# Performance work log

Hardware: AMD Instinct MI355X
Metric: run time of the kernel (lower is better)

## Reference

```python
import jax, jax.numpy as jnp
import numpy as np

B, C, NQ, NK, S, H, FF = 8, 256, 1024, 4096, 16, 8, 2048
DH = C // H
EPS = 1e-5


def _layernorm(x, g, b):
    m = jnp.mean(x, axis=-1, keepdims=True)
    v = jnp.mean((x - m) ** 2, axis=-1, keepdims=True)
    return (x - m) * jax.lax.rsqrt(v + EPS) * g + b


def _box_query(key_pos, query_pos):
    # key_pos: (B,NK,3); query_pos: (B,NQ,6) = centers ++ box sizes (L,H,W)
    centers = query_pos[:, :, None, :3]            # (B,NQ,1,3)
    half = 0.5 * query_pos[:, :, None, 3:]         # (B,NQ,1,3)
    off = jnp.abs(key_pos[:, None, :, :] - centers)  # (B,NQ,NK,3)
    inside = jnp.all(off <= half, axis=-1)         # (B,NQ,NK)
    # first n_sample inside-points in index order (stable sort: inside first)
    order = jnp.argsort(~inside, axis=-1, stable=True)
    idx = order[..., :S]                           # (B,NQ,S)
    valid = jnp.take_along_axis(inside, idx, axis=-1)
    mask = ~valid                                  # True = padded / masked
    idx = jnp.where(mask, 0, idx)
    mask = mask.at[..., 0].set(False)              # matches cuda path: slot 0 never masked
    return idx, mask


def _forward(query, key, query_pos, key_pos,
             q_w, q_b, k_w, k_b, v_w, v_b, o_w, o_b,
             lin1_w, lin1_b, lin2_w, lin2_b,
             n1_g, n1_b, n2_g, n2_b, qpe_w, qpe_b, kpe_w, kpe_b):
    idx, mask = _box_query(key_pos, query_pos)     # (B,NQ,S), (B,NQ,S)
    # gather neighborhoods
    gxyz = jax.vmap(lambda kp, ix: kp[ix])(key_pos, idx)        # (B,NQ,S,3)
    gxyz = gxyz - query_pos[:, :, None, :3]                     # center-relative
    gfeat = jax.vmap(lambda kf, ix: kf[:, ix])(key, idx)        # (B,C,NQ,S)

    BQ = B * NQ
    kfeat = jnp.transpose(gfeat, (0, 2, 3, 1)).reshape(BQ, S, C)   # (BQ,S,C)
    kpe = gxyz.reshape(BQ, S, 3) @ kpe_w.T + kpe_b                 # cross_embed
    qtok = jnp.transpose(query, (0, 2, 1)).reshape(BQ, C)          # (BQ,C)
    qpe = (query_pos @ qpe_w.T + qpe_b).reshape(BQ, C)             # pos_embed

    # multihead cross-attention: 1 query vs S=16 local keys per group
    kv_in = kfeat + kpe
    qh = ((qtok + qpe) @ q_w.T + q_b).reshape(BQ, H, DH)
    kh = (kv_in @ k_w.T + k_b).reshape(BQ, S, H, DH)
    vh = (kv_in @ v_w.T + v_b).reshape(BQ, S, H, DH)
    scores = jnp.einsum('bhd,bshd->bhs', qh, kh) / np.sqrt(DH)    # (BQ,H,S)
    scores = jnp.where(mask.reshape(BQ, 1, S), -1e30, scores)
    attn = jax.nn.softmax(scores, axis=-1)
    ao = jnp.einsum('bhs,bshd->bhd', attn, vh).reshape(BQ, C)
    ao = ao @ o_w.T + o_b

    x = _layernorm(qtok + ao, n1_g, n1_b)                         # post-norm
    ff = jax.nn.relu(x @ lin1_w.T + lin1_b) @ lin2_w.T + lin2_b
    x = _layernorm(x + ff, n2_g, n2_b)
    return jnp.transpose(x.reshape(B, NQ, C), (0, 2, 1))          # (B,C,NQ)


def setup_inputs() -> dict:
    rng = jax.random.key(0)
    ks = jax.random.split(rng, 24)
    s = 0.02
    query = jax.random.normal(ks[0], (B, C, NQ), jnp.float32)
    key = jax.random.normal(ks[1], (B, C, NK), jnp.float32)
    key_pos = jax.random.uniform(ks[2], (B, NK, 3), jnp.float32)
    centers = jax.random.uniform(ks[3], (B, NQ, 3), jnp.float32)
    sizes = jax.random.uniform(ks[4], (B, NQ, 3), jnp.float32, minval=0.1, maxval=0.4)
    query_pos = jnp.concatenate([centers, sizes], axis=-1)
    p = {
        'q_w': jax.random.normal(ks[5], (C, C)) * s, 'q_b': jnp.zeros((C,)),
        'k_w': jax.random.normal(ks[6], (C, C)) * s, 'k_b': jnp.zeros((C,)),
        'v_w': jax.random.normal(ks[7], (C, C)) * s, 'v_b': jnp.zeros((C,)),
        'o_w': jax.random.normal(ks[8], (C, C)) * s, 'o_b': jnp.zeros((C,)),
        'lin1_w': jax.random.normal(ks[9], (FF, C)) * s, 'lin1_b': jnp.zeros((FF,)),
        'lin2_w': jax.random.normal(ks[10], (C, FF)) * s, 'lin2_b': jnp.zeros((C,)),
        'n1_g': jnp.ones((C,)), 'n1_b': jnp.zeros((C,)),
        'n2_g': jnp.ones((C,)), 'n2_b': jnp.zeros((C,)),
        'qpe_w': jax.random.normal(ks[11], (C, 6)) * s, 'qpe_b': jnp.zeros((C,)),
        'kpe_w': jax.random.normal(ks[12], (C, 3)) * s, 'kpe_b': jnp.zeros((C,)),
    }
    return dict(query=query, key=key, query_pos=query_pos, key_pos=key_pos, **p)


def reference(query, key, query_pos, key_pos,
              q_w, q_b, k_w, k_b, v_w, v_b, o_w, o_b,
              lin1_w, lin1_b, lin2_w, lin2_b,
              n1_g, n1_b, n2_g, n2_b, qpe_w, qpe_b, kpe_w, kpe_b):
    return _forward(query, key, query_pos, key_pos,
                    q_w, q_b, k_w, k_b, v_w, v_b, o_w, o_b,
                    lin1_w, lin1_b, lin2_w, lin2_b,
                    n1_g, n1_b, n2_g, n2_b, qpe_w, qpe_b, kpe_w, kpe_b)
```

## Files before the change

### kernel.cpp

```cpp
#include <hip/hip_runtime.h>
#include <cstdint>

#define B_   8
#define C_   256
#define NQ_  1024
#define NK_  4096
#define S_   16
#define H_   8
#define FF_  2048
#define DH_  32
#define BQ_  (B_*NQ_)
#define EPS_ 1e-5f
#define KS_  8

typedef __bf16 bf16x8 __attribute__((ext_vector_type(8)));
typedef __bf16 bf16x4 __attribute__((ext_vector_type(4)));
typedef float  f32x4  __attribute__((ext_vector_type(4)));

struct CvtArgs {
  const float* src[6];
  __bf16* dst[6];
};

#define SEGA 2048
#define SEGB 10240
#define SEGC 12288
#define SEGD 13568
#define NPREP 13584

__global__ __launch_bounds__(256) void k_prep(
    const float* __restrict__ query, const float* __restrict__ key,
    const float* __restrict__ query_pos, const float* __restrict__ key_pos,
    const float* __restrict__ qpe_w, const float* __restrict__ qpe_b,
    const float* __restrict__ k_w, const float* __restrict__ k_b,
    const float* __restrict__ v_w, const float* __restrict__ v_b,
    const float* __restrict__ kpe_w, const float* __restrict__ kpe_b,
    CvtArgs ca,
    __bf16* __restrict__ keyTb, __bf16* __restrict__ qtokb,
    __bf16* __restrict__ qinb,
    float4* __restrict__ Pk, float4* __restrict__ Pv,
    int* __restrict__ idxo, int* __restrict__ masko) {
  __shared__ __align__(16) float smem[1248];
  int blk = blockIdx.x, t = threadIdx.x;
  int tx = t & 31, ty = t >> 5;

  if (blk < SEGA) {
    int lane = t & 63;
    int q = blk * 4 + (t >> 6);
    int b = q >> 10;
    const float* kpb = key_pos + (size_t)b * NK_ * 3;
    const float* qp = query_pos + (size_t)q * 6;
    float cx = qp[0], cy = qp[1], cz = qp[2];
    float hx = 0.5f * qp[3], hy = 0.5f * qp[4], hz = 0.5f * qp[5];
    int* iq = idxo + (size_t)q * S_;
    int found = 0;
    for (int ch = 0; ch < NK_ / 64; ch += 4) {
      float dx[4], dy[4], dz[4];
#pragma unroll
      for (int u = 0; u < 4; ++u) {
        int k = (ch + u) * 64 + lane;
        dx[u] = fabsf(kpb[k * 3 + 0] - cx);
        dy[u] = fabsf(kpb[k * 3 + 1] - cy);
        dz[u] = fabsf(kpb[k * 3 + 2] - cz);
      }
#pragma unroll
      for (int u = 0; u < 4; ++u) {
        bool inside = (dx[u] <= hx) && (dy[u] <= hy) && (dz[u] <= hz);
        unsigned long long bal = __ballot(inside);
        if (inside) {
          int slot = found + __popcll(bal & ((1ull << lane) - 1ull));
          if (slot < S_) iq[slot] = (ch + u) * 64 + lane;
        }
        found += __popcll(bal);
      }
      if (found >= S_) break;
    }
    if (found > S_) found = S_;
    if (lane < S_) {
      int m = (lane < found) ? 0 : 1;
      if (lane >= found) iq[lane] = 0;
      if (lane == 0) m = 0;
      masko[(size_t)q * S_ + lane] = m;
    }
  } else if (blk < SEGB) {
    int local = blk - SEGA;
    float (*tt)[33] = (float(*)[33])smem;
    int x = local & 127, y = (local >> 7) & 7, z = local >> 10;
    int j0 = x * 32, i0 = y * 32;
    const float* inz = key + (size_t)z * C_ * NK_;
    __bf16* outz = keyTb + (size_t)z * NK_ * C_;
#pragma unroll
    for (int r = 0; r < 32; r += 8)
      tt[ty + r][tx] = inz[(size_t)(i0 + ty + r) * NK_ + (j0 + tx)];
    __syncthreads();
#pragma unroll
    for (int r = 0; r < 32; r += 8)
      outz[(size_t)(j0 + ty + r) * C_ + (i0 + tx)] = (__bf16)tt[tx][ty + r];
  } else if (blk < SEGC) {
    int local = blk - SEGB;
    float (*tt)[33] = (float(*)[33])smem;
    float (*sqp)[6] = (float(*)[6])(smem + 1056);
    int x = local & 31, y = (local >> 5) & 7, z = local >> 8;
    int nq0 = x * 32, c0 = y * 32;
    const float* inz = query + (size_t)z * C_ * NQ_;
#pragma unroll
    for (int r = 0; r < 32; r += 8)
      tt[ty + r][tx] = inz[(size_t)(c0 + ty + r) * NQ_ + (nq0 + tx)];
    if (t < 192)
      sqp[t / 6][t % 6] = query_pos[((size_t)z * NQ_ + nq0 + t / 6) * 6 + (t % 6)];
    int c = c0 + tx;
    float w0 = qpe_w[c * 6 + 0], w1 = qpe_w[c * 6 + 1], w2 = qpe_w[c * 6 + 2];
    float w3 = qpe_w[c * 6 + 3], w4 = qpe_w[c * 6 + 4], w5 = qpe_w[c * 6 + 5];
    float wb = qpe_b[c];
    __syncthreads();
#pragma unroll
    for (int r = 0; r < 32; r += 8) {
      int nql = ty + r;
      size_t row = (size_t)z * NQ_ + nq0 + nql;
      float v = tt[tx][nql];
      float pe = wb + sqp[nql][0] * w0 + sqp[nql][1] * w1 + sqp[nql][2] * w2 +
                 sqp[nql][3] * w3 + sqp[nql][4] * w4 + sqp[nql][5] * w5;
      qtokb[row * C_ + c] = (__bf16)v;
      qinb[row * C_ + c] = (__bf16)(v + pe);
    }
  } else if (blk < SEGD) {
    int local = blk - SEGC;
    int idx, base;
    if (local < 64)       { idx = 0; base = local; }
    else if (local < 128) { idx = 1; base = local - 64; }
    else if (local < 192) { idx = 2; base = local - 128; }
    else if (local < 256) { idx = 3; base = local - 192; }
    else if (local < 768) { idx = 4; base = local - 256; }
    else                  { idx = 5; base = local - 768; }
    size_t off = (size_t)base * 1024 + t * 4;
    float4 v = *(const float4*)(ca.src[idx] + off);
    __bf16* o = ca.dst[idx] + off;
    o[0] = (__bf16)v.x; o[1] = (__bf16)v.y; o[2] = (__bf16)v.z; o[3] = (__bf16)v.w;
  } else {
    int local = blk - SEGD;
    int bx = local & 7, bv = local >> 3;
    const float* w  = bv ? v_w : k_w;
    const float* wb = bv ? v_b : k_b;
    float4* P = bv ? Pv : Pk;
    float4 (*red)[8] = (float4(*)[8])smem;
    int nl = t >> 3, ks = (t & 7) * 32;
    int n = bx * 32 + nl;
    const float* wr = w + (size_t)n * C_;
    float p0 = 0.f, p1 = 0.f, p2 = 0.f, pb = 0.f;
#pragma unroll
    for (int k = ks; k < ks + 32; ++k) {
      float wv = wr[k];
      p0 += kpe_w[k * 3 + 0] * wv;
      p1 += kpe_w[k * 3 + 1] * wv;
      p2 += kpe_w[k * 3 + 2] * wv;
      pb += kpe_b[k] * wv;
    }
    red[nl][t & 7] = make_float4(p0, p1, p2, pb);
    __syncthreads();
    if (t < 32) {
      float4 s = red[t][0];
#pragma unroll
      for (int j = 1; j < 8; ++j) {
        float4 r = red[t][j];
        s.x += r.x; s.y += r.y; s.z += r.z; s.w += r.w;
      }
      s.w += wb[bx * 32 + t];
      P[bx * 32 + t] = s;
    }
  }
}

template <int BM, int BN, int RELU, int OUT_BF16>
__device__ __forceinline__ void gemm_body(
    const __bf16* __restrict__ A, const __bf16* __restrict__ Wn,
    const float* __restrict__ bias, void* __restrict__ outp,
    int n0, int m0, int N, int K, int kbeg, int kend) {
  constexpr int MI = BM / 32, JN = BN / 32;
  constexpr int AIT = (BM * 64) / 2048, BIT = (BN * 64) / 2048;
  __shared__ __bf16 As[BM][72];
  __shared__ __bf16 Bs[BN][72];
  int t = threadIdx.x;
  int lane = t & 63, w = t >> 6;
  int lane16 = lane & 15, quad = lane >> 4;
  int wm = (w & 1) * (BM / 2), wn = (w >> 1) * (BN / 2);

  f32x4 acc[MI][JN];
#pragma unroll
  for (int i = 0; i < MI; ++i)
#pragma unroll
    for (int j = 0; j < JN; ++j) acc[i][j] = (f32x4){0.f, 0.f, 0.f, 0.f};

  for (int k0 = kbeg; k0 < kend; k0 += 64) {
#pragma unroll
    for (int i = 0; i < AIT; ++i) {
      int ii = i * 256 + t;
      int m = ii >> 3, kc = (ii & 7) * 8;
      *(bf16x8*)&As[m][kc] = *(const bf16x8*)&A[(size_t)(m0 + m) * K + k0 + kc];
    }
#pragma unroll
    for (int i = 0; i < BIT; ++i) {
      int ii = i * 256 + t;
      int m = ii >> 3, kc = (ii & 7) * 8;
      *(bf16x8*)&Bs[m][kc] = *(const bf16x8*)&Wn[(size_t)(n0 + m) * K + k0 + kc];
    }
    __syncthreads();
#pragma unroll
    for (int kk = 0; kk < 64; kk += 32) {
      bf16x8 af[MI], bfr[JN];
#pragma unroll
      for (int i = 0; i < MI; ++i)
        af[i] = *(const bf16x8*)&As[wm + i * 16 + lane16][kk + quad * 8];
#pragma unroll
      for (int j = 0; j < JN; ++j)
        bfr[j] = *(const bf16x8*)&Bs[wn + j * 16 + lane16][kk + quad * 8];
#pragma unroll
      for (int i = 0; i < MI; ++i)
#pragma unroll
        for (int j = 0; j < JN; ++j)
          acc[i][j] = __builtin_amdgcn_mfma_f32_16x16x32_bf16(af[i], bfr[j], acc[i][j], 0, 0, 0);
    }
    __syncthreads();
  }

#pragma unroll
  for (int j = 0; j < JN; ++j) {
    int col = n0 + wn + j * 16 + lane16;
    float bv = bias ? bias[col] : 0.f;
#pragma unroll
    for (int i = 0; i < MI; ++i) {
#pragma unroll
      for (int r = 0; r < 4; ++r) {
        int row = m0 + wm + i * 16 + quad * 4 + r;
        float v = acc[i][j][r] + bv;
        if (RELU) v = fmaxf(v, 0.f);
        if (OUT_BF16)
          ((__bf16*)outp)[(size_t)row * N + col] = (__bf16)v;
        else
          ((float*)outp)[(size_t)row * N + col] = v;
      }
    }
  }
}

template <int BM, int BN, int RELU, int OUT_BF16>
__global__ __launch_bounds__(256) void k_gemm(
    const __bf16* __restrict__ A, const __bf16* __restrict__ Wn,
    const float* __restrict__ bias, void* __restrict__ outp, int N, int K) {
  gemm_body<BM, BN, RELU, OUT_BF16>(A, Wn, bias, outp,
                                    blockIdx.x * BN, blockIdx.y * BM, N, K, 0, K);
}

__global__ __launch_bounds__(256) void k_gemmsk(
    const __bf16* __restrict__ A, const __bf16* __restrict__ Wn,
    __bf16* __restrict__ partials) {
  int ks = blockIdx.z;
  int kbeg = ks * (FF_ / KS_), kend = kbeg + FF_ / KS_;
  gemm_body<128, 128, 0, 1>(A, Wn, nullptr,
                            partials + (size_t)ks * BQ_ * C_,
                            blockIdx.x * 128, blockIdx.y * 128, C_, FF_, kbeg, kend);
}

__global__ __launch_bounds__(256) void k_gemmsko(
    const __bf16* __restrict__ A, const __bf16* __restrict__ Wn,
    __bf16* __restrict__ partials) {
  int ks = blockIdx.z;
  int kbeg = ks * 128, kend = kbeg + 128;
  gemm_body<128, 64, 0, 1>(A, Wn, nullptr,
                           partials + (size_t)ks * BQ_ * C_,
                           blockIdx.x * 64, blockIdx.y * 128, C_, C_, kbeg, kend);
}

__global__ __launch_bounds__(256) void k_gemm2(
    const __bf16* __restrict__ keyTb, const __bf16* __restrict__ kvwb,
    __bf16* __restrict__ khvbuf,
    const __bf16* __restrict__ qinb, const __bf16* __restrict__ qwb,
    const float* __restrict__ q_b, __bf16* __restrict__ qhb) {
  int blk = blockIdx.x;
  const __bf16 *A, *Wn; const float* bias; __bf16* outp; int n0, m0, N;
  if (blk < 128) {
    A = qinb; Wn = qwb; bias = q_b; outp = qhb;
    n0 = (blk & 1) * 128; m0 = (blk >> 1) * 128; N = 256;
  } else {
    int l = blk - 128;
    A = keyTb; Wn = kvwb; bias = nullptr; outp = khvbuf;
    n0 = (l & 3) * 128; m0 = (l >> 2) * 128; N = 512;
  }
  gemm_body<128, 128, 0, 1>(A, Wn, bias, outp, n0, m0, N, 256, 0, 256);
}

__global__ __launch_bounds__(256) void k_attnf(
    const __bf16* __restrict__ khv,
    const float* __restrict__ key_pos,
    const float* __restrict__ query_pos,
    const int* __restrict__ idx,
    const int* __restrict__ maskb,
    const __bf16* __restrict__ qhb,
    const float4* __restrict__ Pk,
    const float4* __restrict__ Pv,
    __bf16* __restrict__ aob) {
  __shared__ __bf16 kvs[S_][520];
  __shared__ float qrow[C_];
  __shared__ float sc[H_][S_];
  __shared__ float pw[H_][S_];
  __shared__ float4 gx4[S_];
  __shared__ float4 pgxs[H_];
  __shared__ float4 qpks[H_];
  __shared__ int srow[S_], smask[S_];
  int bq = blockIdx.x, b = bq >> 10, t = threadIdx.x;

  if (t < S_) {
    int k = idx[(size_t)bq * S_ + t];
    srow[t] = b * NK_ + k;
    smask[t] = maskb[(size_t)bq * S_ + t];
    const float* kpp = key_pos + ((size_t)b * NK_ + k) * 3;
    const float* qp  = query_pos + (size_t)bq * 6;
    gx4[t] = make_float4(kpp[0] - qp[0], kpp[1] - qp[1], kpp[2] - qp[2], 1.f);
  }
  float qv_t = (float)qhb[(size_t)bq * C_ + t];
  qrow[t] = qv_t;
  {
    float4 p = Pk[t];
    p.x *= qv_t; p.y *= qv_t; p.z *= qv_t; p.w *= qv_t;
#pragma unroll
    for (int off = 16; off >= 1; off >>= 1) {
      p.x += __shfl_xor(p.x, off);
      p.y += __shfl_xor(p.y, off);
      p.z += __shfl_xor(p.z, off);
      p.w += __shfl_xor(p.w, off);
    }
    if ((t & 31) == 0) {
      const float s = 0.17677669529663687f;
      qpks[t >> 5] = make_float4(p.x * s, p.y * s, p.z * s, p.w * s);
    }
  }
  __syncthreads();
  {
    int s = t >> 4, c0 = (t & 15) * 32;
    const __bf16* src = khv + (size_t)srow[s] * 512 + c0;
    *(bf16x8*)&kvs[s][c0]      = *(const bf16x8*)&src[0];
    *(bf16x8*)&kvs[s][c0 + 8]  = *(const bf16x8*)&src[8];
    *(bf16x8*)&kvs[s][c0 + 16] = *(const bf16x8*)&src[16];
    *(bf16x8*)&kvs[s][c0 + 24] = *(const bf16x8*)&src[24];
  }
  __syncthreads();
  if (t < H_ * S_) {
    int h = t >> 4, s = t & (S_ - 1);
    float d = 0.f;
#pragma unroll
    for (int c0 = 0; c0 < 32; c0 += 8) {
      bf16x8 xv = *(const bf16x8*)&kvs[s][h * 32 + c0];
#pragma unroll
      for (int j = 0; j < 8; ++j) d += qrow[h * 32 + c0 + j] * (float)xv[j];
    }
    d *= 0.17677669529663687f;
    float4 g = gx4[s];
    float4 pk = qpks[h];
    d += g.x * pk.x + g.y * pk.y + g.z * pk.z + pk.w;
    if (smask[s]) d = -1e30f;
    sc[h][s] = d;
  }
  __syncthreads();
  if (t < H_) {
    float mx = -3.4e38f;
#pragma unroll
    for (int s = 0; s < S_; ++s) mx = fmaxf(mx, sc[t][s]);
    float e[S_], sum = 0.f;
#pragma unroll
    for (int s = 0; s < S_; ++s) { e[s] = expf(sc[t][s] - mx); sum += e[s]; }
    float inv = 1.f / sum;
    float gxx = 0.f, gyy = 0.f, gzz = 0.f;
#pragma unroll
    for (int s = 0; s < S_; ++s) {
      float p = e[s] * inv;
      pw[t][s] = p;
      float4 g = gx4[s];
      gxx += p * g.x; gyy += p * g.y; gzz += p * g.z;
    }
    pgxs[t] = make_float4(gxx, gyy, gzz, 1.f);
  }
  __syncthreads();
  {
    int h = t >> 5;
    float a = 0.f;
#pragma unroll
    for (int s = 0; s < S_; ++s) a += pw[h][s] * (float)kvs[s][256 + t];
    float4 pv = Pv[t];
    float4 g = pgxs[h];
    a += g.x * pv.x + g.y * pv.y + g.z * pv.z + pv.w;
    aob[(size_t)bq * C_ + t] = (__bf16)a;
  }
}

__global__ __launch_bounds__(256) void k_ln1(const __bf16* __restrict__ xa,
                                             const __bf16* __restrict__ op2,
                                             const float* __restrict__ obias,
                                             const float* __restrict__ g,
                                             const float* __restrict__ bb,
                                             __bf16* __restrict__ outb) {
  int wid = (blockIdx.x * 256 + threadIdx.x) >> 6;
  int lane = threadIdx.x & 63;
  bf16x4 va = *(const bf16x4*)&xa[(size_t)wid * C_ + lane * 4];
  float4 ob4 = *(const float4*)(obias + lane * 4);
  bf16x4 p0 = *(const bf16x4*)&op2[(size_t)wid * C_ + lane * 4];
  bf16x4 p1 = *(const bf16x4*)&op2[(size_t)BQ_ * C_ + (size_t)wid * C_ + lane * 4];
  float x0 = (float)va[0] + ob4.x + (float)p0[0] + (float)p1[0];
  float x1 = (float)va[1] + ob4.y + (float)p0[1] + (float)p1[1];
  float x2 = (float)va[2] + ob4.z + (float)p0[2] + (float)p1[2];
  float x3 = (float)va[3] + ob4.w + (float)p0[3] + (float)p1[3];
  float s = x0 + x1 + x2 + x3;
#pragma unroll
  for (int off = 32; off >= 1; off >>= 1) s += __shfl_xor(s, off);
  float mean = s * (1.f / C_);
  float d0 = x0 - mean, d1 = x1 - mean, d2 = x2 - mean, d3 = x3 - mean;
  float v = d0 * d0 + d1 * d1 + d2 * d2 + d3 * d3;
#pragma unroll
  for (int off = 32; off >= 1; off >>= 1) v += __shfl_xor(v, off);
  float inv = 1.f / sqrtf(v * (1.f / C_) + EPS_);
  float4 g4 = *(const float4*)(g + lane * 4);
  float4 b4 = *(const float4*)(bb + lane * 4);
  __bf16* obp = outb + (size_t)wid * C_ + lane * 4;
  obp[0] = (__bf16)(d0 * inv * g4.x + b4.x);
  obp[1] = (__bf16)(d1 * inv * g4.y + b4.y);
  obp[2] = (__bf16)(d2 * inv * g4.z + b4.z);
  obp[3] = (__bf16)(d3 * inv * g4.w + b4.w);
}

__global__ __launch_bounds__(256) void k_lnt(const __bf16* __restrict__ x1b,
                                             const __bf16* __restrict__ ff2p,
                                             const float* __restrict__ l2bias,
                                             const float* __restrict__ g,
                                             const float* __restrict__ bb,
                                             float* __restrict__ out) {
  __shared__ float buf[32][257];
  int z = blockIdx.y, nq0 = blockIdx.x * 32;
  int t = threadIdx.x;
  int w = t >> 6, lane = t & 63;
  float4 g4 = *(const float4*)(g + lane * 4);
  float4 b4 = *(const float4*)(bb + lane * 4);
  float4 l2b = *(const float4*)(l2bias + lane * 4);
#pragma unroll
  for (int rr = 0; rr < 8; ++rr) {
    int row = w * 8 + rr;
    size_t grow = (size_t)z * NQ_ + nq0 + row;
    bf16x4 va = *(const bf16x4*)&x1b[grow * C_ + lane * 4];
    float x0 = (float)va[0] + l2b.x, x1 = (float)va[1] + l2b.y;
    float x2 = (float)va[2] + l2b.z, x3 = (float)va[3] + l2b.w;
#pragma unroll
    for (int ks = 0; ks < KS_; ++ks) {
      bf16x4 p = *(const bf16x4*)&ff2p[((size_t)ks * BQ_ + grow) * C_ + lane * 4];
      x0 += (float)p[0]; x1 += (float)p[1]; x2 += (float)p[2]; x3 += (float)p[3];
    }
    float s = x0 + x1 + x2 + x3;
#pragma unroll
    for (int off = 32; off >= 1; off >>= 1) s += __shfl_xor(s, off);
    float mean = s * (1.f / C_);
    float d0 = x0 - mean, d1 = x1 - mean, d2 = x2 - mean, d3 = x3 - mean;
    float v = d0 * d0 + d1 * d1 + d2 * d2 + d3 * d3;
#pragma unroll
    for (int off = 32; off >= 1; off >>= 1) v += __shfl_xor(v, off);
    float inv = 1.f / sqrtf(v * (1.f / C_) + EPS_);
    buf[row][lane * 4 + 0] = d0 * inv * g4.x + b4.x;
    buf[row][lane * 4 + 1] = d1 * inv * g4.y + b4.y;
    buf[row][lane * 4 + 2] = d2 * inv * g4.z + b4.z;
    buf[row][lane * 4 + 3] = d3 * inv * g4.w + b4.w;
  }
  __syncthreads();
  int tx = t & 31, ty = t >> 5;
#pragma unroll
  for (int ci = 0; ci < 32; ++ci) {
    int c = ci * 8 + ty;
    out[((size_t)z * C_ + c) * NQ_ + nq0 + tx] = buf[tx][c];
  }
}

extern "C" void kernel_launch(void* const* d_in, const int* in_sizes, int n_in,
                              void* d_out, int out_size, void* d_ws, size_t ws_size,
                              hipStream_t stream) {
  const float* query     = (const float*)d_in[0];
  const float* key       = (const float*)d_in[1];
  const float* query_pos = (const float*)d_in[2];
  const float* key_pos   = (const float*)d_in[3];
  const float* q_w = (const float*)d_in[4];  const float* q_b = (const float*)d_in[5];
  const float* k_w = (const float*)d_in[6];  const float* k_b = (const float*)d_in[7];
  const float* v_w = (const float*)d_in[8];  const float* v_b = (const float*)d_in[9];
  const float* o_w = (const float*)d_in[10]; const float* o_b = (const float*)d_in[11];
  const float* lin1_w = (const float*)d_in[12]; const float* lin1_b = (const float*)d_in[13];
  const float* lin2_w = (const float*)d_in[14]; const float* lin2_b = (const float*)d_in[15];
  const float* n1_g = (const float*)d_in[16]; const float* n1_b = (const float*)d_in[17];
  const float* n2_g = (const float*)d_in[18]; const float* n2_b = (const float*)d_in[19];
  const float* qpe_w = (const float*)d_in[20]; const float* qpe_b = (const float*)d_in[21];
  const float* kpe_w = (const float*)d_in[22]; const float* kpe_b = (const float*)d_in[23];
  float* out = (float*)d_out;

  const size_t BQc = (size_t)BQ_ * C_;
  float* w = (float*)d_ws;
  size_t o = 0;
  __bf16* keyTb = (__bf16*)(w + o); o += (size_t)B_ * NK_ * C_ / 2;
  __bf16* qtokb = (__bf16*)(w + o); o += BQc / 2;
  __bf16* op2  = (__bf16*)(w + o); o += BQc;
  __bf16* khvbuf = (__bf16*)(w + o); o += (size_t)B_ * NK_ * 512 / 2;
  __bf16* ff2p = (__bf16*)(w + o); o += BQc * KS_ / 2;
  __bf16* qinb = (__bf16*)(w + o); o += BQc / 2;
  __bf16* qhb  = (__bf16*)(w + o); o += BQc / 2;
  __bf16* aob  = (__bf16*)(w + o); o += BQc / 2;
  __bf16* x1b  = (__bf16*)(w + o); o += BQc / 2;
  __bf16* qwb  = (__bf16*)(w + o); o += (size_t)C_ * C_ / 2;
  __bf16* kvwb = (__bf16*)(w + o); o += (size_t)C_ * C_;
  __bf16* owb  = (__bf16*)(w + o); o += (size_t)C_ * C_ / 2;
  __bf16* l1b  = (__bf16*)(w + o); o += (size_t)C_ * FF_ / 2;
  __bf16* l2b  = (__bf16*)(w + o); o += (size_t)C_ * FF_ / 2;
  float4* Pk   = (float4*)(w + o); o += C_ * 4;
  float4* Pv   = (float4*)(w + o); o += C_ * 4;
  int* idxb  = (int*)(w + o); o += (size_t)BQ_ * S_;
  int* maskb = (int*)(w + o); o += (size_t)BQ_ * S_;
  __bf16* ff1b = khvbuf;

  CvtArgs ca;
  ca.src[0] = q_w; ca.dst[0] = qwb;
  ca.src[1] = k_w; ca.dst[1] = kvwb;
  ca.src[2] = v_w; ca.dst[2] = kvwb + (size_t)C_ * C_;
  ca.src[3] = o_w; ca.dst[3] = owb;
  ca.src[4] = lin1_w; ca.dst[4] = l1b;
  ca.src[5] = lin2_w; ca.dst[5] = l2b;
  k_prep<<<NPREP, 256, 0, stream>>>(query, key, query_pos, key_pos,
                                    qpe_w, qpe_b, k_w, k_b, v_w, v_b,
                                    kpe_w, kpe_b, ca,
                                    keyTb, qtokb, qinb, Pk, Pv, idxb, maskb);
  k_gemm2<<<128 + 1024, 256, 0, stream>>>(keyTb, kvwb, khvbuf, qinb, qwb, q_b, qhb);
  k_attnf<<<BQ_, 256, 0, stream>>>(khvbuf, key_pos, query_pos, idxb, maskb,
                                   qhb, Pk, Pv, aob);
  k_gemmsko<<<dim3(C_ / 64, BQ_ / 128, 2), 256, 0, stream>>>(aob, owb, op2);
  k_ln1<<<BQ_ / 4, 256, 0, stream>>>(qtokb, op2, o_b, n1_g, n1_b, x1b);
  k_gemm<128, 128, 1, 1><<<dim3(FF_ / 128, BQ_ / 128), 256, 0, stream>>>(
      x1b, l1b, lin1_b, ff1b, FF_, C_);
  k_gemmsk<<<dim3(C_ / 128, BQ_ / 128, KS_), 256, 0, stream>>>(ff1b, l2b, ff2p);
  k_lnt<<<dim3(NQ_ / 32, B_), 256, 0, stream>>>(x1b, ff2p, lin2_b, n2_g, n2_b, out);
}
```

Measured before the change: 259.5 us.

## Fuse split-K GEMM reductions with LayerNorm via last-block atomic counters

Merges the output-projection split-K GEMM with the first LayerNorm, and the FF2 split-K GEMM with the final LayerNorm plus transpose. Each row tile counts finished split blocks with an atomic counter, and the last block to finish reduces the partials and applies the norm. This removes two kernel launches and their inter-kernel gaps. In exchange, the norm work for each row tile now runs serially in a single block, which reduces parallelism in the tail and adds fences and atomics.

```diff
diff --git a/kernel.cpp b/kernel.cpp
--- a/kernel.cpp
+++ b/kernel.cpp
@@ -26,7 +26,8 @@
 #define SEGB 10240
 #define SEGC 12288
 #define SEGD 13568
-#define NPREP 13584
+#define SEGE 13584
+#define NPREP 13585
 
 __global__ __launch_bounds__(256) void k_prep(
     const float* __restrict__ query, const float* __restrict__ key,
@@ -39,7 +40,8 @@
     __bf16* __restrict__ keyTb, __bf16* __restrict__ qtokb,
     __bf16* __restrict__ qinb,
     float4* __restrict__ Pk, float4* __restrict__ Pv,
-    int* __restrict__ idxo, int* __restrict__ masko) {
+    int* __restrict__ idxo, int* __restrict__ masko,
+    int* __restrict__ cnts) {
   __shared__ __align__(16) float smem[1248];
   int blk = blockIdx.x, t = threadIdx.x;
   int tx = t & 31, ty = t >> 5;
@@ -136,7 +138,7 @@
     float4 v = *(const float4*)(ca.src[idx] + off);
     __bf16* o = ca.dst[idx] + off;
     o[0] = (__bf16)v.x; o[1] = (__bf16)v.y; o[2] = (__bf16)v.z; o[3] = (__bf16)v.w;
-  } else {
+  } else if (blk < SEGE) {
     int local = blk - SEGD;
     int bx = local & 7, bv = local >> 3;
     const float* w  = bv ? v_w : k_w;
@@ -167,18 +169,19 @@
       s.w += wb[bx * 32 + t];
       P[bx * 32 + t] = s;
     }
+  } else {
+    if (t < 128) cnts[t] = 0;
   }
 }
 
 template <int BM, int BN, int RELU, int OUT_BF16>
-__device__ __forceinline__ void gemm_body(
+__device__ __forceinline__ void gemm_core(
+    __bf16 (*As)[72], __bf16 (*Bs)[72],
     const __bf16* __restrict__ A, const __bf16* __restrict__ Wn,
     const float* __restrict__ bias, void* __restrict__ outp,
     int n0, int m0, int N, int K, int kbeg, int kend) {
   constexpr int MI = BM / 32, JN = BN / 32;
   constexpr int AIT = (BM * 64) / 2048, BIT = (BN * 64) / 2048;
-  __shared__ __bf16 As[BM][72];
-  __shared__ __bf16 Bs[BN][72];
   int t = threadIdx.x;
   int lane = t & 63, w = t >> 6;
   int lane16 = lane & 15, quad = lane >> 4;
@@ -243,31 +246,21 @@
 }
 
 template <int BM, int BN, int RELU, int OUT_BF16>
+__device__ __forceinline__ void gemm_body(
+    const __bf16* __restrict__ A, const __bf16* __restrict__ Wn,
+    const float* __restrict__ bias, void* __restrict__ outp,
+    int n0, int m0, int N, int K, int kbeg, int kend) {
+  __shared__ __bf16 As[BM][72];
+  __shared__ __bf16 Bs[BN][72];
+  gemm_core<BM, BN, RELU, OUT_BF16>(As, Bs, A, Wn, bias, outp, n0, m0, N, K, kbeg, kend);
+}
+
+template <int BM, int BN, int RELU, int OUT_BF16>
 __global__ __launch_bounds__(256) void k_gemm(
     const __bf16* __restrict__ A, const __bf16* __restrict__ Wn,
     const float* __restrict__ bias, void* __restrict__ outp, int N, int K) {
   gemm_body<BM, BN, RELU, OUT_BF16>(A, Wn, bias, outp,
                                     blockIdx.x * BN, blockIdx.y * BM, N, K, 0, K);
-}
-
-__global__ __launch_bounds__(256) void k_gemmsk(
-    const __bf16* __restrict__ A, const __bf16* __restrict__ Wn,
-    __bf16* __restrict__ partials) {
-  int ks = blockIdx.z;
-  int kbeg = ks * (FF_ / KS_), kend = kbeg + FF_ / KS_;
-  gemm_body<128, 128, 0, 1>(A, Wn, nullptr,
-                            partials + (size_t)ks * BQ_ * C_,
-                            blockIdx.x * 128, blockIdx.y * 128, C_, FF_, kbeg, kend);
-}
-
-__global__ __launch_bounds__(256) void k_gemmsko(
-    const __bf16* __restrict__ A, const __bf16* __restrict__ Wn,
-    __bf16* __restrict__ partials) {
-  int ks = blockIdx.z;
-  int kbeg = ks * 128, kend = kbeg + 128;
-  gemm_body<128, 64, 0, 1>(A, Wn, nullptr,
-                           partials + (size_t)ks * BQ_ * C_,
-                           blockIdx.x * 64, blockIdx.y * 128, C_, C_, kbeg, kend);
 }
 
 __global__ __launch_bounds__(256) void k_gemm2(
@@ -286,6 +279,125 @@
     n0 = (l & 3) * 128; m0 = (l >> 2) * 128; N = 512;
   }
   gemm_body<128, 128, 0, 1>(A, Wn, bias, outp, n0, m0, N, 256, 0, 256);
+}
+
+__global__ __launch_bounds__(256) void k_oproj_ln1(
+    const __bf16* __restrict__ aob, const __bf16* __restrict__ owb,
+    __bf16* __restrict__ op2,
+    const __bf16* __restrict__ qtokb, const float* __restrict__ obias,
+    const float* __restrict__ g, const float* __restrict__ bb,
+    __bf16* __restrict__ x1b, int* __restrict__ cnt) {
+  __shared__ __align__(16) char smem[(128 + 64) * 72 * 2];
+  __bf16 (*As)[72] = (__bf16(*)[72])smem;
+  __bf16 (*Bs)[72] = (__bf16(*)[72])(smem + 128 * 72 * 2);
+  __shared__ int lastf;
+  int ks = blockIdx.z;
+  int m0 = blockIdx.y * 128;
+  gemm_core<128, 64, 0, 1>(As, Bs, aob, owb, nullptr,
+                           op2 + (size_t)ks * BQ_ * C_,
+                           blockIdx.x * 64, m0, C_, C_, ks * 128, ks * 128 + 128);
+  __threadfence();
+  int t = threadIdx.x;
+  if (t == 0) lastf = (atomicAdd(&cnt[blockIdx.y], 1) == 7);
+  __syncthreads();
+  if (!lastf) return;
+  __threadfence();
+  int lane = t & 63;
+  float4 ob4 = *(const float4*)(obias + lane * 4);
+  float4 g4 = *(const float4*)(g + lane * 4);
+  float4 b4 = *(const float4*)(bb + lane * 4);
+  for (int rr = 0; rr < 32; ++rr) {
+    int wid = m0 + rr * 4 + (t >> 6);
+    bf16x4 va = *(const bf16x4*)&qtokb[(size_t)wid * C_ + lane * 4];
+    bf16x4 p0 = *(const bf16x4*)&op2[(size_t)wid * C_ + lane * 4];
+    bf16x4 p1 = *(const bf16x4*)&op2[(size_t)BQ_ * C_ + (size_t)wid * C_ + lane * 4];
+    float x0 = (float)va[0] + ob4.x + (float)p0[0] + (float)p1[0];
+    float x1 = (float)va[1] + ob4.y + (float)p0[1] + (float)p1[1];
+    float x2 = (float)va[2] + ob4.z + (float)p0[2] + (float)p1[2];
+    float x3 = (float)va[3] + ob4.w + (float)p0[3] + (float)p1[3];
+    float s = x0 + x1 + x2 + x3;
+#pragma unroll
+    for (int off = 32; off >= 1; off >>= 1) s += __shfl_xor(s, off);
+    float mean = s * (1.f / C_);
+    float d0 = x0 - mean, d1 = x1 - mean, d2 = x2 - mean, d3 = x3 - mean;
+    float v = d0 * d0 + d1 * d1 + d2 * d2 + d3 * d3;
+#pragma unroll
+    for (int off = 32; off >= 1; off >>= 1) v += __shfl_xor(v, off);
+    float inv = 1.f / sqrtf(v * (1.f / C_) + EPS_);
+    __bf16* obp = x1b + (size_t)wid * C_ + lane * 4;
+    obp[0] = (__bf16)(d0 * inv * g4.x + b4.x);
+    obp[1] = (__bf16)(d1 * inv * g4.y + b4.y);
+    obp[2] = (__bf16)(d2 * inv * g4.z + b4.z);
+    obp[3] = (__bf16)(d3 * inv * g4.w + b4.w);
+  }
+}
+
+__global__ __launch_bounds__(256) void k_ff2_lnt(
+    const __bf16* __restrict__ ff1b, const __bf16* __restrict__ l2w,
+    __bf16* __restrict__ ff2p,
+    const __bf16* __restrict__ x1b, const float* __restrict__ l2bias,
+    const float* __restrict__ g, const float* __restrict__ bb,
+    float* __restrict__ out, int* __restrict__ cnt) {
+  __shared__ __align__(16) char smem[2 * 128 * 72 * 2];
+  __bf16 (*As)[72] = (__bf16(*)[72])smem;
+  __bf16 (*Bs)[72] = (__bf16(*)[72])(smem + 128 * 72 * 2);
+  __shared__ int lastf;
+  int ks = blockIdx.z;
+  int m0 = blockIdx.y * 128;
+  gemm_core<128, 128, 0, 1>(As, Bs, ff1b, l2w, nullptr,
+                            ff2p + (size_t)ks * BQ_ * C_,
+                            blockIdx.x * 128, m0, C_, FF_,
+                            ks * (FF_ / KS_), (ks + 1) * (FF_ / KS_));
+  __threadfence();
+  int t = threadIdx.x;
+  if (t == 0) lastf = (atomicAdd(&cnt[blockIdx.y], 1) == 15);
+  __syncthreads();
+  if (!lastf) return;
+  __threadfence();
+  float (*buf)[257] = (float(*)[257])smem;
+  int z = m0 >> 10;
+  int nqbase = m0 & (NQ_ - 1);
+  int w = t >> 6, lane = t & 63;
+  float4 g4 = *(const float4*)(g + lane * 4);
+  float4 b4 = *(const float4*)(bb + lane * 4);
+  float4 l2b = *(const float4*)(l2bias + lane * 4);
+  for (int sub = 0; sub < 4; ++sub) {
+    int nq0 = nqbase + sub * 32;
+    __syncthreads();
+#pragma unroll
+    for (int rr = 0; rr < 8; ++rr) {
+      int row = w * 8 + rr;
+      size_t grow = (size_t)z * NQ_ + nq0 + row;
+      bf16x4 va = *(const bf16x4*)&x1b[grow * C_ + lane * 4];
+      float x0 = (float)va[0] + l2b.x, x1 = (float)va[1] + l2b.y;
+      float x2 = (float)va[2] + l2b.z, x3 = (float)va[3] + l2b.w;
+#pragma unroll
+      for (int kk = 0; kk < KS_; ++kk) {
+        bf16x4 p = *(const bf16x4*)&ff2p[((size_t)kk * BQ_ + grow) * C_ + lane * 4];
+        x0 += (float)p[0]; x1 += (float)p[1]; x2 += (float)p[2]; x3 += (float)p[3];
+      }
+      float s = x0 + x1 + x2 + x3;
+#pragma unroll
+      for (int off = 32; off >= 1; off >>= 1) s += __shfl_xor(s, off);
+      float mean = s * (1.f / C_);
+      float d0 = x0 - mean, d1 = x1 - mean, d2 = x2 - mean, d3 = x3 - mean;
+      float v = d0 * d0 + d1 * d1 + d2 * d2 + d3 * d3;
+#pragma unroll
+      for (int off = 32; off >= 1; off >>= 1) v += __shfl_xor(v, off);
+      float inv = 1.f / sqrtf(v * (1.f / C_) + EPS_);
+      buf[row][lane * 4 + 0] = d0 * inv * g4.x + b4.x;
+      buf[row][lane * 4 + 1] = d1 * inv * g4.y + b4.y;
+      buf[row][lane * 4 + 2] = d2 * inv * g4.z + b4.z;
+      buf[row][lane * 4 + 3] = d3 * inv * g4.w + b4.w;
+    }
+    __syncthreads();
+    int tx = t & 31, ty = t >> 5;
+#pragma unroll
+    for (int ci = 0; ci < 32; ++ci) {
+      int c = ci * 8 + ty;
+      out[((size_t)z * C_ + c) * NQ_ + nq0 + tx] = buf[tx][c];
+    }
+  }
 }
 
 __global__ __launch_bounds__(256) void k_attnf(
@@ -388,88 +500,6 @@
     float4 g = pgxs[h];
     a += g.x * pv.x + g.y * pv.y + g.z * pv.z + pv.w;
     aob[(size_t)bq * C_ + t] = (__bf16)a;
-  }
-}
-
-__global__ __launch_bounds__(256) void k_ln1(const __bf16* __restrict__ xa,
-                                             const __bf16* __restrict__ op2,
-                                             const float* __restrict__ obias,
-                                             const float* __restrict__ g,
-                                             const float* __restrict__ bb,
-                                             __bf16* __restrict__ outb) {
-  int wid = (blockIdx.x * 256 + threadIdx.x) >> 6;
-  int lane = threadIdx.x & 63;
-  bf16x4 va = *(const bf16x4*)&xa[(size_t)wid * C_ + lane * 4];
-  float4 ob4 = *(const float4*)(obias + lane * 4);
-  bf16x4 p0 = *(const bf16x4*)&op2[(size_t)wid * C_ + lane * 4];
-  bf16x4 p1 = *(const bf16x4*)&op2[(size_t)BQ_ * C_ + (size_t)wid * C_ + lane * 4];
-  float x0 = (float)va[0] + ob4.x + (float)p0[0] + (float)p1[0];
-  float x1 = (float)va[1] + ob4.y + (float)p0[1] + (float)p1[1];
-  float x2 = (float)va[2] + ob4.z + (float)p0[2] + (float)p1[2];
-  float x3 = (float)va[3] + ob4.w + (float)p0[3] + (float)p1[3];
-  float s = x0 + x1 + x2 + x3;
-#pragma unroll
-  for (int off = 32; off >= 1; off >>= 1) s += __shfl_xor(s, off);
-  float mean = s * (1.f / C_);
-  float d0 = x0 - mean, d1 = x1 - mean, d2 = x2 - mean, d3 = x3 - mean;
-  float v = d0 * d0 + d1 * d1 + d2 * d2 + d3 * d3;
-#pragma unroll
-  for (int off = 32; off >= 1; off >>= 1) v += __shfl_xor(v, off);
-  float inv = 1.f / sqrtf(v * (1.f / C_) + EPS_);
-  float4 g4 = *(const float4*)(g + lane * 4);
-  float4 b4 = *(const float4*)(bb + lane * 4);
-  __bf16* obp = outb + (size_t)wid * C_ + lane * 4;
-  obp[0] = (__bf16)(d0 * inv * g4.x + b4.x);
-  obp[1] = (__bf16)(d1 * inv * g4.y + b4.y);
-  obp[2] = (__bf16)(d2 * inv * g4.z + b4.z);
-  obp[3] = (__bf16)(d3 * inv * g4.w + b4.w);
-}
-
-__global__ __launch_bounds__(256) void k_lnt(const __bf16* __restrict__ x1b,
-                                             const __bf16* __restrict__ ff2p,
-                                             const float* __restrict__ l2bias,
-                                             const float* __restrict__ g,
-                                             const float* __restrict__ bb,
-                                             float* __restrict__ out) {
-  __shared__ float buf[32][257];
-  int z = blockIdx.y, nq0 = blockIdx.x * 32;
-  int t = threadIdx.x;
-  int w = t >> 6, lane = t & 63;
-  float4 g4 = *(const float4*)(g + lane * 4);
-  float4 b4 = *(const float4*)(bb + lane * 4);
-  float4 l2b = *(const float4*)(l2bias + lane * 4);
-#pragma unroll
-  for (int rr = 0; rr < 8; ++rr) {
-    int row = w * 8 + rr;
-    size_t grow = (size_t)z * NQ_ + nq0 + row;
-    bf16x4 va = *(const bf16x4*)&x1b[grow * C_ + lane * 4];
-    float x0 = (float)va[0] + l2b.x, x1 = (float)va[1] + l2b.y;
-    float x2 = (float)va[2] + l2b.z, x3 = (float)va[3] + l2b.w;
-#pragma unroll
-    for (int ks = 0; ks < KS_; ++ks) {
-      bf16x4 p = *(const bf16x4*)&ff2p[((size_t)ks * BQ_ + grow) * C_ + lane * 4];
-      x0 += (float)p[0]; x1 += (float)p[1]; x2 += (float)p[2]; x3 += (float)p[3];
-    }
-    float s = x0 + x1 + x2 + x3;
-#pragma unroll
-    for (int off = 32; off >= 1; off >>= 1) s += __shfl_xor(s, off);
-    float mean = s * (1.f / C_);
-    float d0 = x0 - mean, d1 = x1 - mean, d2 = x2 - mean, d3 = x3 - mean;
-    float v = d0 * d0 + d1 * d1 + d2 * d2 + d3 * d3;
-#pragma unroll
-    for (int off = 32; off >= 1; off >>= 1) v += __shfl_xor(v, off);
-    float inv = 1.f / sqrtf(v * (1.f / C_) + EPS_);
-    buf[row][lane * 4 + 0] = d0 * inv * g4.x + b4.x;
-    buf[row][lane * 4 + 1] = d1 * inv * g4.y + b4.y;
-    buf[row][lane * 4 + 2] = d2 * inv * g4.z + b4.z;
-    buf[row][lane * 4 + 3] = d3 * inv * g4.w + b4.w;
-  }
-  __syncthreads();
-  int tx = t & 31, ty = t >> 5;
-#pragma unroll
-  for (int ci = 0; ci < 32; ++ci) {
-    int c = ci * 8 + ty;
-    out[((size_t)z * C_ + c) * NQ_ + nq0 + tx] = buf[tx][c];
   }
 }
 
@@ -513,6 +543,7 @@
   float4* Pv   = (float4*)(w + o); o += C_ * 4;
   int* idxb  = (int*)(w + o); o += (size_t)BQ_ * S_;
   int* maskb = (int*)(w + o); o += (size_t)BQ_ * S_;
+  int* cnts  = (int*)(w + o); o += 128;
   __bf16* ff1b = khvbuf;
 
   CvtArgs ca;
@@ -525,14 +556,14 @@
   k_prep<<<NPREP, 256, 0, stream>>>(query, key, query_pos, key_pos,
                                     qpe_w, qpe_b, k_w, k_b, v_w, v_b,
                                     kpe_w, kpe_b, ca,
-                                    keyTb, qtokb, qinb, Pk, Pv, idxb, maskb);
+                                    keyTb, qtokb, qinb, Pk, Pv, idxb, maskb, cnts);
   k_gemm2<<<128 + 1024, 256, 0, stream>>>(keyTb, kvwb, khvbuf, qinb, qwb, q_b, qhb);
   k_attnf<<<BQ_, 256, 0, stream>>>(khvbuf, key_pos, query_pos, idxb, maskb,
                                    qhb, Pk, Pv, aob);
-  k_gemmsko<<<dim3(C_ / 64, BQ_ / 128, 2), 256, 0, stream>>>(aob, owb, op2);
-  k_ln1<<<BQ_ / 4, 256, 0, stream>>>(qtokb, op2, o_b, n1_g, n1_b, x1b);
+  k_oproj_ln1<<<dim3(C_ / 64, BQ_ / 128, 2), 256, 0, stream>>>(
+      aob, owb, op2, qtokb, o_b, n1_g, n1_b, x1b, cnts);
   k_gemm<128, 128, 1, 1><<<dim3(FF_ / 128, BQ_ / 128), 256, 0, stream>>>(
       x1b, l1b, lin1_b, ff1b, FF_, C_);
-  k_gemmsk<<<dim3(C_ / 128, BQ_ / 128, KS_), 256, 0, stream>>>(ff1b, l2b, ff2p);
-  k_lnt<<<dim3(NQ_ / 32, B_), 256, 0, stream>>>(x1b, ff2p, lin2_b, n2_g, n2_b, out);
-}
+  k_ff2_lnt<<<dim3(C_ / 128, BQ_ / 128, KS_), 256, 0, stream>>>(
+      ff1b, l2b, ff2p, x1b, lin2_b, n2_g, n2_b, out, cnts + 64);
+}
```

Result: slower. 549.2 us (+111.6%).
